# Performance work log

Measured on AMD Instinct MI355X. Metric: run time of the kernel, lower is better.

Reference implementation:

```python
import jax, jax.numpy as jnp
import numpy as np

INPUT_DIM = 64
LATENT_DIM = 512
K = 32
BATCH = 262144


def xavier_uniform(key, shape):
    fan_out, fan_in = shape
    limit = float(np.sqrt(6.0 / (fan_in + fan_out)))
    return jax.random.uniform(key, shape, jnp.float32, -limit, limit)


def setup_inputs() -> dict:
    key = jax.random.key(0)
    kx, ke, kd = jax.random.split(key, 3)
    x = jax.random.normal(kx, (BATCH, INPUT_DIM), dtype=jnp.float32)
    enc_W = xavier_uniform(ke, (LATENT_DIM, INPUT_DIM))  # torch Linear weight layout [out, in]
    enc_b = jnp.zeros((LATENT_DIM,), jnp.float32)
    dec_W = xavier_uniform(kd, (INPUT_DIM, LATENT_DIM))
    dec_b = jnp.zeros((INPUT_DIM,), jnp.float32)
    return {"x": x, "enc_W": enc_W, "enc_b": enc_b, "dec_W": dec_W, "dec_b": dec_b}


def reference(x, enc_W, enc_b, dec_W, dec_b):
    # encode: linear -> relu -> top-k mask
    z = jax.nn.relu(x @ enc_W.T + enc_b)                 # [B, LATENT_DIM]
    vals, idx = jax.lax.top_k(z, K)                      # [B, K]
    rows = jnp.arange(z.shape[0])[:, None]               # [B, 1]
    z_sparse = jnp.zeros_like(z).at[rows, idx].set(vals) # scatter top-k back
    # decode
    x_hat = z_sparse @ dec_W.T + dec_b                   # [B, INPUT_DIM]
    return x_hat, z_sparse
```

## Files before the change

### kernel.cpp

```cpp
#include <hip/hip_runtime.h>


#define BATCH 262144
#define IND   64
#define LAT   512
#define TOPK  32
#define RPB   128
#define TR    32
#define NTT   (RPB / TR)
#define CCAP  64
#define EPSC  3.5e-5f
#define NB    32
#define NBPAD 36

typedef __attribute__((ext_vector_type(8))) short short8;
typedef __attribute__((ext_vector_type(4))) float f32x4;

__device__ __forceinline__ unsigned short f2bf(float f) {
  unsigned u = __float_as_uint(f);
  unsigned r = ((u >> 16) & 1u) + 0x7FFFu;
  return (unsigned short)((u + r) >> 16);
}
__device__ __forceinline__ float bfbits2f(unsigned short s) {
  return __uint_as_float(((unsigned)s) << 16);
}
__device__ __forceinline__ float edgef(int t) {
  return __uint_as_float((unsigned)(1888 + t) << 19);
}
__device__ __forceinline__ short8 pack8(float4 a, float4 b) {
  short8 r;
  r[0] = (short)f2bf(a.x); r[1] = (short)f2bf(a.y);
  r[2] = (short)f2bf(a.z); r[3] = (short)f2bf(a.w);
  r[4] = (short)f2bf(b.x); r[5] = (short)f2bf(b.y);
  r[6] = (short)f2bf(b.z); r[7] = (short)f2bf(b.w);
  return r;
}
__device__ __forceinline__ void split8(const float* p, short8& h, short8& l) {
  #pragma unroll
  for (int i = 0; i < 8; i++) {
    float v = p[i];
    unsigned short hb = f2bf(v);
    float r = v - bfbits2f(hb);
    h[i] = (short)hb;
    l[i] = (short)f2bf(r);
  }
}

__global__ __launch_bounds__(256)
__attribute__((amdgpu_waves_per_eu(2, 2)))
void sae_fused(const float* __restrict__ xg,
               const float* __restrict__ encW,
               const float* __restrict__ encB,
               const float* __restrict__ decW,
               const float* __restrict__ decB,
               float* __restrict__ out_xhat,
               float* __restrict__ out_z)
{
  __shared__ unsigned       hist[TR][NBPAD];
  __shared__ unsigned       fb[256];
  __shared__ unsigned short zsp[TR][520];
  __shared__ float    xtile[TR][68];
  __shared__ float    cval[TR][CCAP];
  __shared__ unsigned short cidx[TR][CCAP];
  __shared__ float    rowlo[TR];
  __shared__ float    rowep[TR];
  __shared__ float    xabs[TR];
  __shared__ float    xlo0[TR];
  __shared__ float    xinvw[TR];
  __shared__ float    xwid[TR];
  __shared__ int      ccnt[TR];
  __shared__ int      degen[TR];
  __shared__ int      wmax_i;
  __shared__ int      fbmask;

  const int tid  = threadIdx.x;
  const int w    = tid >> 6;
  const int lane = tid & 63;
  const int c    = lane & 15;
  const int q    = lane >> 4;

  if (tid == 0) wmax_i = 0;
  __syncthreads();

  short8 beh[8][2], bel[8][2];
  float  lmax = 0.0f;
  #pragma unroll
  for (int n = 0; n < 8; n++)
    #pragma unroll
    for (int ks = 0; ks < 2; ks++) {
      const float* p = encW + (size_t)(128*w + 16*n + c)*IND + 32*ks + 8*q;
      #pragma unroll
      for (int i = 0; i < 8; i++) lmax = fmaxf(lmax, fabsf(p[i]));
      split8(p, beh[n][ks], bel[n][ks]);
    }
  atomicMax(&wmax_i, __float_as_int(lmax));

  float ebias[8];
  #pragma unroll
  for (int n = 0; n < 8; n++) ebias[n] = encB[128*w + 16*n + c];
  const float dbias = decB[16*w + c];
  __syncthreads();
  const float wmaxf = __int_as_float(wmax_i);

  #pragma unroll 1
  for (int t = 0; t < NTT; t++) {
    const int rowbase = blockIdx.x * RPB + t * TR;

    {
      uint4 z4 = {0,0,0,0};
      uint4* hp = (uint4*)&hist[0][0];
      hp[tid] = z4;
      if (tid < 32) hp[256 + tid] = z4;
      uint4* zp = (uint4*)&zsp[0][0];
      #pragma unroll
      for (int i = 0; i < 8; i++) zp[tid + 256*i] = z4;
      if (tid < 32) zp[2048 + tid] = z4;
      if (tid < TR) { ccnt[tid] = 0; degen[tid] = 0; }
      if (tid == 0) fbmask = 0;
    }
    {
      const int row = tid >> 3, sub = tid & 7;
      const f32x4* gp = (const f32x4*)(xg + (size_t)(rowbase + row)*IND) + 2*sub;
      f32x4 a = __builtin_nontemporal_load(gp);
      f32x4 b = __builtin_nontemporal_load(gp + 1);
      *(f32x4*)&xtile[row][8*sub]     = a;
      *(f32x4*)&xtile[row][8*sub + 4] = b;
      float s  = fabsf(a.x)+fabsf(a.y)+fabsf(a.z)+fabsf(a.w)
               + fabsf(b.x)+fabsf(b.y)+fabsf(b.z)+fabsf(b.w);
      float s2 = a.x*a.x+a.y*a.y+a.z*a.z+a.w*a.w
               + b.x*b.x+b.y*b.y+b.z*b.z+b.w*b.w;
      s  += __shfl_xor(s, 1);  s  += __shfl_xor(s, 2);  s  += __shfl_xor(s, 4);
      s2 += __shfl_xor(s2, 1); s2 += __shfl_xor(s2, 2); s2 += __shfl_xor(s2, 4);
      if (sub == 0) {
        xabs[row] = s;
        const float sig = 0.058926f * sqrtf(s2);
        xlo0[row]  = fmaxf(0.7f * sig, edgef(1));
        xwid[row]  = (2.5f / (float)NB) * sig;
        xinvw[row] = (float)NB / fmaxf(2.5f * sig, 1e-20f);
      }
    }
    __syncthreads();

    f32x4 acc[2][8];
    #pragma unroll
    for (int m2 = 0; m2 < 2; m2++)
      #pragma unroll
      for (int n = 0; n < 8; n++) acc[m2][n] = (f32x4){0.f,0.f,0.f,0.f};

    #pragma unroll
    for (int m2 = 0; m2 < 2; m2++) {
      const float* xr = &xtile[16*m2 + c][0];
      short8 a0h, a0l, a1h, a1l;
      split8(xr + 8*q,      a0h, a0l);
      split8(xr + 32 + 8*q, a1h, a1l);
      #pragma unroll
      for (int n = 0; n < 8; n++) {
        acc[m2][n] = __builtin_amdgcn_mfma_f32_16x16x32_bf16(a0h, beh[n][0], acc[m2][n], 0,0,0);
        acc[m2][n] = __builtin_amdgcn_mfma_f32_16x16x32_bf16(a0l, beh[n][0], acc[m2][n], 0,0,0);
        acc[m2][n] = __builtin_amdgcn_mfma_f32_16x16x32_bf16(a0h, bel[n][0], acc[m2][n], 0,0,0);
        acc[m2][n] = __builtin_amdgcn_mfma_f32_16x16x32_bf16(a1h, beh[n][1], acc[m2][n], 0,0,0);
        acc[m2][n] = __builtin_amdgcn_mfma_f32_16x16x32_bf16(a1l, beh[n][1], acc[m2][n], 0,0,0);
        acc[m2][n] = __builtin_amdgcn_mfma_f32_16x16x32_bf16(a1h, bel[n][1], acc[m2][n], 0,0,0);
      }
    }
    {
      float flo[2][4], fiw[2][4];
      #pragma unroll
      for (int m2 = 0; m2 < 2; m2++)
        #pragma unroll
        for (int r = 0; r < 4; r++) {
          flo[m2][r] = xlo0[16*m2 + 4*q + r];
          fiw[m2][r] = xinvw[16*m2 + 4*q + r];
        }
      #pragma unroll
      for (int m2 = 0; m2 < 2; m2++)
        #pragma unroll
        for (int n = 0; n < 8; n++)
          #pragma unroll
          for (int r = 0; r < 4; r++) {
            float v = fmaxf(acc[m2][n][r] + ebias[n], 0.0f);
            acc[m2][n][r] = v;
            if (v >= flo[m2][r]) {
              const int row = 16*m2 + 4*q + r;
              int k = (int)((v - flo[m2][r]) * fiw[m2][r]);
              k = min(k, NB-1);
              atomicAdd(&hist[row][k], 1u);
            }
          }
    }
    __syncthreads();

    #pragma unroll 1
    for (int rr = 0; rr < 8; rr++) {
      const int row = 8*w + rr;
      uint4 h = {0,0,0,0};
      if (lane < 8) h = *(const uint4*)&hist[row][4*lane];
      int T = (int)(h.x + h.y + h.z + h.w);
      int I = T;
      #pragma unroll
      for (int d = 1; d < 8; d <<= 1) {
        int t2 = __shfl_down(I, d);
        if (lane + d < 8) I += t2;
      }
      const int I0 = __shfl(I, 0);
      if (I0 < TOPK) {
        if (lane == 0) atomicOr(&fbmask, (int)(1u << row));
      } else {
        unsigned long long msk = __ballot(I >= TOPK);
        const int ls = __popcll(msk) - 1;
        const int Il = __shfl(I, ls);
        const int hx = __shfl((int)h.x, ls);
        const int hy = __shfl((int)h.y, ls);
        const int hz = __shfl((int)h.z, ls);
        const int s1 = Il - hx, s2 = s1 - hy, s3 = s2 - hz;
        const int t8 = (s3 >= TOPK) ? 4*ls+3 : (s2 >= TOPK) ? 4*ls+2
                     : (s1 >= TOPK) ? 4*ls+1 : 4*ls;
        if (lane == 0) {
          const float eps2 = EPSC * wmaxf * xabs[row] + 1e-7f;
          rowep[row] = eps2;
          rowlo[row] = fmaxf(xlo0[row] + (float)t8 * xwid[row] - 2.0f*eps2, 1e-30f);
        }
      }
    }
    __syncthreads();

    if (fbmask) {
      unsigned fbm = (unsigned)fbmask;
      while (fbm) {
        const int R = (int)__ffs(fbm) - 1;
        fbm &= fbm - 1;
        fb[tid] = 0;
        __syncthreads();
        if ((lane >> 4) == ((R >> 2) & 3)) {
          const int m2R = R >> 4, rR = R & 3;
          #pragma unroll
          for (int m2 = 0; m2 < 2; m2++)
            #pragma unroll
            for (int r = 0; r < 4; r++)
              if (m2 == m2R && r == rR) {
                #pragma unroll
                for (int n = 0; n < 8; n++) {
                  float v = acc[m2][n][r];
                  int k8 = (int)(__float_as_uint(v) >> 19) - 1888;
                  k8 = max(0, min(255, k8));
                  atomicAdd(&fb[k8], 1u);
                }
              }
        }
        __syncthreads();
        if (w == 0) {
          uint4 h = *(const uint4*)&fb[4*lane];
          int T = (int)(h.x + h.y + h.z + h.w);
          int I = T;
          #pragma unroll
          for (int d = 1; d < 64; d <<= 1) {
            int t2 = __shfl_down(I, d);
            if (lane + d < 64) I += t2;
          }
          const int I0  = __shfl(I, 0);
          const int hx0 = __shfl((int)h.x, 0);
          if (I0 - hx0 < TOPK) {
            if (lane == 0) { degen[R] = 1; rowlo[R] = edgef(1); rowep[R] = 0.f; }
          } else {
            unsigned long long msk = __ballot(I >= TOPK);
            const int ls = __popcll(msk) - 1;
            const int Il = __shfl(I, ls);
            const int hx = __shfl((int)h.x, ls);
            const int hy = __shfl((int)h.y, ls);
            const int hz = __shfl((int)h.z, ls);
            const int s1 = Il - hx, s2 = s1 - hy, s3 = s2 - hz;
            const int t8 = (s3 >= TOPK) ? 4*ls+3 : (s2 >= TOPK) ? 4*ls+2
                         : (s1 >= TOPK) ? 4*ls+1 : 4*ls;
            if (lane == 0) {
              const float eps2 = EPSC * wmaxf * xabs[R] + 1e-7f;
              rowep[R] = eps2;
              rowlo[R] = fmaxf(edgef(t8) - 2.0f*eps2, 1e-30f);
            }
          }
        }
        __syncthreads();
      }
    }

    #pragma unroll
    for (int m2 = 0; m2 < 2; m2++)
      #pragma unroll
      for (int r = 0; r < 4; r++) {
        const int row = 16*m2 + 4*q + r;
        const float lo = rowlo[row];
        const int dg = degen[row];
        #pragma unroll
        for (int n = 0; n < 8; n++) {
          const float v = acc[m2][n][r];
          if (v >= lo) {
            if (dg) {
              zsp[row][128*w + 16*n + c] = f2bf(v);
            } else {
              int slot = atomicAdd(&ccnt[row], 1);
              if (slot < CCAP) {
                cval[row][slot] = v;
                cidx[row][slot] = (unsigned short)(128*w + 16*n + c);
              }
            }
          }
        }
      }
    __syncthreads();

    #pragma unroll 1
    for (int rr = 0; rr < 8; rr++) {
      const int row = 8*w + rr;
      if (!degen[row]) {
        const int m = min(ccnt[row], CCAP);
        float cv = (lane < m) ? cval[row][lane] : -1e30f;
        int   ci = (lane < m) ? (int)cidx[row][lane] : 0x7FFFFFFF;
        int rank = 0;
        for (int jj = 0; jj < m; jj++) {
          const float vj = __shfl(cv, jj);
          const int   ij = __shfl(ci, jj);
          rank += (vj > cv || (vj == cv && ij < ci)) ? 1 : 0;
        }
        bool kept = (lane < m) && (rank < TOPK);
        float kv = kept ? cv : 1e30f;
        float uv = (!kept && lane < m) ? cv : -1e30f;
        #pragma unroll
        for (int d = 1; d < 64; d <<= 1) {
          kv = fminf(kv, __shfl_xor(kv, d));
          uv = fmaxf(uv, __shfl_xor(uv, d));
        }
        if (kv - uv < 2.0f*rowep[row]) {
          const int js = (lane < m) ? ci : 0;
          const float* wr = encW + (size_t)js * IND;
          const float* xr = &xtile[row][0];
          float s = 0.0f;
          #pragma unroll 1
          for (int g4 = 0; g4 < 4; g4++) {
            const float4 w0 = *(const float4*)(wr + 16*g4);
            const float4 w1 = *(const float4*)(wr + 16*g4 + 4);
            const float4 w2 = *(const float4*)(wr + 16*g4 + 8);
            const float4 w3 = *(const float4*)(wr + 16*g4 + 12);
            const float* xk = xr + 16*g4;
            s = fmaf(xk[0],  w0.x, s); s = fmaf(xk[1],  w0.y, s);
            s = fmaf(xk[2],  w0.z, s); s = fmaf(xk[3],  w0.w, s);
            s = fmaf(xk[4],  w1.x, s); s = fmaf(xk[5],  w1.y, s);
            s = fmaf(xk[6],  w1.z, s); s = fmaf(xk[7],  w1.w, s);
            s = fmaf(xk[8],  w2.x, s); s = fmaf(xk[9],  w2.y, s);
            s = fmaf(xk[10], w2.z, s); s = fmaf(xk[11], w2.w, s);
            s = fmaf(xk[12], w3.x, s); s = fmaf(xk[13], w3.y, s);
            s = fmaf(xk[14], w3.z, s); s = fmaf(xk[15], w3.w, s);
          }
          s += encB[js];
          s = fmaxf(s, 0.0f);
          const float val = (lane < m) ? s : -1e30f;
          rank = 0;
          for (int jj = 0; jj < m; jj++) {
            const float vj = __shfl(val, jj);
            const int   ij = __shfl(ci, jj);
            rank += (vj > val || (vj == val && ij < ci)) ? 1 : 0;
          }
          kept = (lane < m) && (rank < TOPK);
          cv = val;
        }
        if (kept) zsp[row][ci] = f2bf(cv);
      }
    }
    __syncthreads();

    #pragma unroll 1
    for (int rr = 0; rr < 8; rr++) {
      const int row = 8*w + rr;
      const unsigned short* zr = &zsp[row][8*lane];
      f32x4 o0, o1;
      o0.x = bfbits2f(zr[0]); o0.y = bfbits2f(zr[1]); o0.z = bfbits2f(zr[2]); o0.w = bfbits2f(zr[3]);
      o1.x = bfbits2f(zr[4]); o1.y = bfbits2f(zr[5]); o1.z = bfbits2f(zr[6]); o1.w = bfbits2f(zr[7]);
      f32x4* orow = (f32x4*)(out_z + (size_t)(rowbase + row)*LAT + 8*lane);
      __builtin_nontemporal_store(o0, orow);
      __builtin_nontemporal_store(o1, orow + 1);
    }
    {
      short8 bd[16];
      #pragma unroll
      for (int ks = 0; ks < 16; ks++) {
        const float* p = decW + (size_t)(16*w + c)*LAT + 32*ks + 8*q;
        bd[ks] = pack8(*(const float4*)p, *(const float4*)(p + 4));
      }
      f32x4 acc2[2];
      acc2[0] = (f32x4){0.f,0.f,0.f,0.f};
      acc2[1] = (f32x4){0.f,0.f,0.f,0.f};
      #pragma unroll
      for (int ks = 0; ks < 16; ks++) {
        short8 a0 = *(const short8*)&zsp[c][32*ks + 8*q];
        short8 a1 = *(const short8*)&zsp[16 + c][32*ks + 8*q];
        acc2[0] = __builtin_amdgcn_mfma_f32_16x16x32_bf16(a0, bd[ks], acc2[0], 0,0,0);
        acc2[1] = __builtin_amdgcn_mfma_f32_16x16x32_bf16(a1, bd[ks], acc2[1], 0,0,0);
      }
      #pragma unroll
      for (int m2 = 0; m2 < 2; m2++)
        #pragma unroll
        for (int r = 0; r < 4; r++)
          out_xhat[(size_t)(rowbase + 16*m2 + 4*q + r)*IND + 16*w + c] = acc2[m2][r] + dbias;
    }
    __syncthreads();
  }
}

extern "C" void kernel_launch(void* const* d_in, const int* in_sizes, int n_in,
                              void* d_out, int out_size, void* d_ws, size_t ws_size,
                              hipStream_t stream) {
  (void)in_sizes; (void)n_in; (void)out_size; (void)d_ws; (void)ws_size;
  const float* x    = (const float*)d_in[0];
  const float* encW = (const float*)d_in[1];
  const float* encB = (const float*)d_in[2];
  const float* decW = (const float*)d_in[3];
  const float* decB = (const float*)d_in[4];
  float* out_xhat = (float*)d_out;
  float* out_z    = out_xhat + (size_t)BATCH * IND;

  dim3 grid(BATCH / RPB), block(256);
  sae_fused<<<grid, block, 0, stream>>>(x, encW, encB, decW, decB, out_xhat, out_z);
}
```

Baseline: 1.786 ms.

## Drop weight low-part MFMAs, always refine boundary candidates exactly, hoist decoder weights

The encoder GEMM drops the low-order bf16 split of the weights, cutting MFMAs per tile from six to four. To absorb the larger approximation error, the candidate margin is widened and capacity doubled. Every boundary candidate is now recomputed with an exact fp32 dot product and re-ranked, instead of only when the gap is ambiguous. Decoder weight packing is hoisted out of the tile loop into registers, trading register pressure for fewer per-tile global loads, and some shared arrays are removed or aliased.

```diff
diff --git a/kernel.cpp b/kernel.cpp
--- a/kernel.cpp
+++ b/kernel.cpp
@@ -8,8 +8,8 @@
 #define RPB   128
 #define TR    32
 #define NTT   (RPB / TR)
-#define CCAP  64
-#define EPSC  3.5e-5f
+#define CCAP  128
+#define EPSC  4.2e-3f
 #define NB    32
 #define NBPAD 36
 
@@ -45,9 +45,41 @@
     l[i] = (short)f2bf(r);
   }
 }
-
-__global__ __launch_bounds__(256)
-__attribute__((amdgpu_waves_per_eu(2, 2)))
+__device__ __forceinline__ float exact_dot64(const float* __restrict__ wr,
+                                             const float* xr) {
+  float s = 0.0f;
+  #pragma unroll 1
+  for (int g = 0; g < 2; g++) {
+    const float4 w0 = *(const float4*)(wr + 32*g);
+    const float4 w1 = *(const float4*)(wr + 32*g + 4);
+    const float4 w2 = *(const float4*)(wr + 32*g + 8);
+    const float4 w3 = *(const float4*)(wr + 32*g + 12);
+    const float4 w4 = *(const float4*)(wr + 32*g + 16);
+    const float4 w5 = *(const float4*)(wr + 32*g + 20);
+    const float4 w6 = *(const float4*)(wr + 32*g + 24);
+    const float4 w7 = *(const float4*)(wr + 32*g + 28);
+    const float* xk = xr + 32*g;
+    s = fmaf(xk[0],  w0.x, s); s = fmaf(xk[1],  w0.y, s);
+    s = fmaf(xk[2],  w0.z, s); s = fmaf(xk[3],  w0.w, s);
+    s = fmaf(xk[4],  w1.x, s); s = fmaf(xk[5],  w1.y, s);
+    s = fmaf(xk[6],  w1.z, s); s = fmaf(xk[7],  w1.w, s);
+    s = fmaf(xk[8],  w2.x, s); s = fmaf(xk[9],  w2.y, s);
+    s = fmaf(xk[10], w2.z, s); s = fmaf(xk[11], w2.w, s);
+    s = fmaf(xk[12], w3.x, s); s = fmaf(xk[13], w3.y, s);
+    s = fmaf(xk[14], w3.z, s); s = fmaf(xk[15], w3.w, s);
+    s = fmaf(xk[16], w4.x, s); s = fmaf(xk[17], w4.y, s);
+    s = fmaf(xk[18], w4.z, s); s = fmaf(xk[19], w4.w, s);
+    s = fmaf(xk[20], w5.x, s); s = fmaf(xk[21], w5.y, s);
+    s = fmaf(xk[22], w5.z, s); s = fmaf(xk[23], w5.w, s);
+    s = fmaf(xk[24], w6.x, s); s = fmaf(xk[25], w6.y, s);
+    s = fmaf(xk[26], w6.z, s); s = fmaf(xk[27], w6.w, s);
+    s = fmaf(xk[28], w7.x, s); s = fmaf(xk[29], w7.y, s);
+    s = fmaf(xk[30], w7.z, s); s = fmaf(xk[31], w7.w, s);
+  }
+  return s;
+}
+
+__global__ __launch_bounds__(256, 2)
 void sae_fused(const float* __restrict__ xg,
                const float* __restrict__ encW,
                const float* __restrict__ encB,
@@ -57,13 +89,10 @@
                float* __restrict__ out_z)
 {
   __shared__ unsigned       hist[TR][NBPAD];
-  __shared__ unsigned       fb[256];
   __shared__ unsigned short zsp[TR][520];
   __shared__ float    xtile[TR][68];
-  __shared__ float    cval[TR][CCAP];
   __shared__ unsigned short cidx[TR][CCAP];
   __shared__ float    rowlo[TR];
-  __shared__ float    rowep[TR];
   __shared__ float    xabs[TR];
   __shared__ float    xlo0[TR];
   __shared__ float    xinvw[TR];
@@ -82,18 +111,29 @@
   if (tid == 0) wmax_i = 0;
   __syncthreads();
 
-  short8 beh[8][2], bel[8][2];
+  short8 beh[8][2];
   float  lmax = 0.0f;
   #pragma unroll
   for (int n = 0; n < 8; n++)
     #pragma unroll
     for (int ks = 0; ks < 2; ks++) {
       const float* p = encW + (size_t)(128*w + 16*n + c)*IND + 32*ks + 8*q;
-      #pragma unroll
-      for (int i = 0; i < 8; i++) lmax = fmaxf(lmax, fabsf(p[i]));
-      split8(p, beh[n][ks], bel[n][ks]);
+      float4 a = *(const float4*)p, b = *(const float4*)(p + 4);
+      lmax = fmaxf(lmax, fmaxf(fmaxf(fabsf(a.x), fabsf(a.y)), fmaxf(fabsf(a.z), fabsf(a.w))));
+      lmax = fmaxf(lmax, fmaxf(fmaxf(fabsf(b.x), fabsf(b.y)), fmaxf(fabsf(b.z), fabsf(b.w))));
+      beh[n][ks] = pack8(a, b);
     }
   atomicMax(&wmax_i, __float_as_int(lmax));
+
+  short8 bd[16];
+  #pragma unroll 1
+  for (int g = 0; g < 4; g++)
+    #pragma unroll
+    for (int j = 0; j < 4; j++) {
+      const int ks = 4*g + j;
+      const float* p = decW + (size_t)(16*w + c)*LAT + 32*ks + 8*q;
+      bd[ks] = pack8(*(const float4*)p, *(const float4*)(p + 4));
+    }
 
   float ebias[8];
   #pragma unroll
@@ -157,10 +197,8 @@
       for (int n = 0; n < 8; n++) {
         acc[m2][n] = __builtin_amdgcn_mfma_f32_16x16x32_bf16(a0h, beh[n][0], acc[m2][n], 0,0,0);
         acc[m2][n] = __builtin_amdgcn_mfma_f32_16x16x32_bf16(a0l, beh[n][0], acc[m2][n], 0,0,0);
-        acc[m2][n] = __builtin_amdgcn_mfma_f32_16x16x32_bf16(a0h, bel[n][0], acc[m2][n], 0,0,0);
         acc[m2][n] = __builtin_amdgcn_mfma_f32_16x16x32_bf16(a1h, beh[n][1], acc[m2][n], 0,0,0);
         acc[m2][n] = __builtin_amdgcn_mfma_f32_16x16x32_bf16(a1l, beh[n][1], acc[m2][n], 0,0,0);
-        acc[m2][n] = __builtin_amdgcn_mfma_f32_16x16x32_bf16(a1h, bel[n][1], acc[m2][n], 0,0,0);
       }
     }
     {
@@ -217,7 +255,6 @@
                      : (s1 >= TOPK) ? 4*ls+1 : 4*ls;
         if (lane == 0) {
           const float eps2 = EPSC * wmaxf * xabs[row] + 1e-7f;
-          rowep[row] = eps2;
           rowlo[row] = fmaxf(xlo0[row] + (float)t8 * xwid[row] - 2.0f*eps2, 1e-30f);
         }
       }
@@ -225,6 +262,7 @@
     __syncthreads();
 
     if (fbmask) {
+      unsigned* fb = &hist[0][0];
       unsigned fbm = (unsigned)fbmask;
       while (fbm) {
         const int R = (int)__ffs(fbm) - 1;
@@ -260,7 +298,7 @@
           const int I0  = __shfl(I, 0);
           const int hx0 = __shfl((int)h.x, 0);
           if (I0 - hx0 < TOPK) {
-            if (lane == 0) { degen[R] = 1; rowlo[R] = edgef(1); rowep[R] = 0.f; }
+            if (lane == 0) { degen[R] = 1; rowlo[R] = edgef(1); }
           } else {
             unsigned long long msk = __ballot(I >= TOPK);
             const int ls = __popcll(msk) - 1;
@@ -273,7 +311,6 @@
                          : (s1 >= TOPK) ? 4*ls+1 : 4*ls;
             if (lane == 0) {
               const float eps2 = EPSC * wmaxf * xabs[R] + 1e-7f;
-              rowep[R] = eps2;
               rowlo[R] = fmaxf(edgef(t8) - 2.0f*eps2, 1e-30f);
             }
           }
@@ -297,10 +334,7 @@
               zsp[row][128*w + 16*n + c] = f2bf(v);
             } else {
               int slot = atomicAdd(&ccnt[row], 1);
-              if (slot < CCAP) {
-                cval[row][slot] = v;
-                cidx[row][slot] = (unsigned short)(128*w + 16*n + c);
-              }
+              if (slot < CCAP) cidx[row][slot] = (unsigned short)(128*w + 16*n + c);
             }
           }
         }
@@ -310,59 +344,44 @@
     #pragma unroll 1
     for (int rr = 0; rr < 8; rr++) {
       const int row = 8*w + rr;
-      if (!degen[row]) {
-        const int m = min(ccnt[row], CCAP);
-        float cv = (lane < m) ? cval[row][lane] : -1e30f;
-        int   ci = (lane < m) ? (int)cidx[row][lane] : 0x7FFFFFFF;
-        int rank = 0;
-        for (int jj = 0; jj < m; jj++) {
-          const float vj = __shfl(cv, jj);
-          const int   ij = __shfl(ci, jj);
-          rank += (vj > cv || (vj == cv && ij < ci)) ? 1 : 0;
-        }
-        bool kept = (lane < m) && (rank < TOPK);
-        float kv = kept ? cv : 1e30f;
-        float uv = (!kept && lane < m) ? cv : -1e30f;
-        #pragma unroll
-        for (int d = 1; d < 64; d <<= 1) {
-          kv = fminf(kv, __shfl_xor(kv, d));
-          uv = fmaxf(uv, __shfl_xor(uv, d));
-        }
-        if (kv - uv < 2.0f*rowep[row]) {
-          const int js = (lane < m) ? ci : 0;
-          const float* wr = encW + (size_t)js * IND;
-          const float* xr = &xtile[row][0];
-          float s = 0.0f;
-          #pragma unroll 1
-          for (int g4 = 0; g4 < 4; g4++) {
-            const float4 w0 = *(const float4*)(wr + 16*g4);
-            const float4 w1 = *(const float4*)(wr + 16*g4 + 4);
-            const float4 w2 = *(const float4*)(wr + 16*g4 + 8);
-            const float4 w3 = *(const float4*)(wr + 16*g4 + 12);
-            const float* xk = xr + 16*g4;
-            s = fmaf(xk[0],  w0.x, s); s = fmaf(xk[1],  w0.y, s);
-            s = fmaf(xk[2],  w0.z, s); s = fmaf(xk[3],  w0.w, s);
-            s = fmaf(xk[4],  w1.x, s); s = fmaf(xk[5],  w1.y, s);
-            s = fmaf(xk[6],  w1.z, s); s = fmaf(xk[7],  w1.w, s);
-            s = fmaf(xk[8],  w2.x, s); s = fmaf(xk[9],  w2.y, s);
-            s = fmaf(xk[10], w2.z, s); s = fmaf(xk[11], w2.w, s);
-            s = fmaf(xk[12], w3.x, s); s = fmaf(xk[13], w3.y, s);
-            s = fmaf(xk[14], w3.z, s); s = fmaf(xk[15], w3.w, s);
-          }
-          s += encB[js];
-          s = fmaxf(s, 0.0f);
-          const float val = (lane < m) ? s : -1e30f;
-          rank = 0;
-          for (int jj = 0; jj < m; jj++) {
-            const float vj = __shfl(val, jj);
-            const int   ij = __shfl(ci, jj);
-            rank += (vj > val || (vj == val && ij < ci)) ? 1 : 0;
-          }
-          kept = (lane < m) && (rank < TOPK);
-          cv = val;
-        }
-        if (kept) zsp[row][ci] = f2bf(cv);
-      }
+      if (degen[row]) continue;
+      const int m  = min(ccnt[row], CCAP);
+      const int mA = min(m, 64);
+      const int mB = m - mA;
+      const float* xr = &xtile[row][0];
+
+      int ciA = 0xFFFF; float sA = -1e30f;
+      {
+        const int js = (lane < mA) ? (int)cidx[row][lane] : 0;
+        float s = exact_dot64(encW + (size_t)js * IND, xr);
+        s += encB[js];
+        s = fmaxf(s, 0.0f);
+        if (lane < mA) { sA = s; ciA = js; }
+      }
+      int ciB = 0xFFFF; float sB = -1e30f;
+      if (mB > 0) {
+        const int js = (lane < mB) ? (int)cidx[row][64 + lane] : 0;
+        float s = exact_dot64(encW + (size_t)js * IND, xr);
+        s += encB[js];
+        s = fmaxf(s, 0.0f);
+        if (lane < mB) { sB = s; ciB = js; }
+      }
+
+      int rank0 = 0, rank1 = 0;
+      for (int jj = 0; jj < mA; jj++) {
+        const float vj = __shfl(sA, jj);
+        const int   ij = __shfl(ciA, jj);
+        rank0 += (vj > sA || (vj == sA && ij < ciA)) ? 1 : 0;
+        rank1 += (vj > sB || (vj == sB && ij < ciB)) ? 1 : 0;
+      }
+      for (int jj = 0; jj < mB; jj++) {
+        const float vj = __shfl(sB, jj);
+        const int   ij = __shfl(ciB, jj);
+        rank0 += (vj > sA || (vj == sA && ij < ciA)) ? 1 : 0;
+        rank1 += (vj > sB || (vj == sB && ij < ciB)) ? 1 : 0;
+      }
+      if (lane < mA && rank0 < TOPK) zsp[row][ciA] = f2bf(sA);
+      if (mB > 0 && lane < mB && rank1 < TOPK) zsp[row][ciB] = f2bf(sB);
     }
     __syncthreads();
 
@@ -378,12 +397,6 @@
       __builtin_nontemporal_store(o1, orow + 1);
     }
     {
-      short8 bd[16];
-      #pragma unroll
-      for (int ks = 0; ks < 16; ks++) {
-        const float* p = decW + (size_t)(16*w + c)*LAT + 32*ks + 8*q;
-        bd[ks] = pack8(*(const float4*)p, *(const float4*)(p + 4));
-      }
       f32x4 acc2[2];
       acc2[0] = (f32x4){0.f,0.f,0.f,0.f};
       acc2[1] = (f32x4){0.f,0.f,0.f,0.f};
```

Measured after the change: 1.649 ms. -7.7%, faster.
